# Optimization experiments

Measured on AMD Instinct MI355X. Metric: run time of the kernel, lower is better.

The kernel has to match this reference:

```python
import jax, jax.numpy as jnp
import numpy as np

B = 128                      # num_graphs (cell lines per batch)
SIZES = [706, 512, 256, 128] # nodes per graph at each level; final_node = 128
DIM = 256                    # dim_cell
DEG = 8                      # avg degree of gene-gene network
EPS = 1e-5                   # BatchNorm eps


def _build_graph():
    """Build per-graph edges (incl. self-loops, as GATConv adds) and predefined
    cluster assignments per layer, coarsening edges exactly like PyG max_pool
    (remove self-loops + coalesce). Replicated across B graphs with offsets."""
    rng = np.random.default_rng(0)
    e = rng.integers(0, SIZES[0], size=(2, SIZES[0] * DEG))
    e = e[:, e[0] != e[1]]
    e = np.unique(e, axis=1)
    edges, clusters = [], []
    cur = e
    for i in range(3):
        n_cur, n_next = SIZES[i], SIZES[i + 1]
        sl = np.arange(n_cur)
        e_sl = np.concatenate([cur, np.stack([sl, sl])], axis=1)  # add self-loops
        off = np.arange(B) * n_cur
        eg = (e_sl[:, None, :] + off[None, :, None]).reshape(2, -1)
        edges.append(eg.astype(np.int32))
        cl = np.concatenate([np.arange(n_next), rng.integers(0, n_next, size=n_cur - n_next)])
        rng.shuffle(cl)  # surjective cluster assignment n_cur -> n_next
        clg = (cl[None, :] + (np.arange(B) * n_next)[:, None]).reshape(-1)
        clusters.append(clg.astype(np.int32))
        src, dst = cl[cur[0]], cl[cur[1]]
        m = src != dst                      # pool_edge: remove self-loops
        cur = np.unique(np.stack([src[m], dst[m]]), axis=1)  # coalesce
    return edges, clusters


def setup_inputs() -> dict:
    edges, clusters = _build_graph()
    key = jax.random.key(0)
    ks = jax.random.split(key, 16)
    d = {"x": jax.random.normal(ks[0], (B * SIZES[0], 3), jnp.float32)}
    ins = [3, DIM, DIM]
    for i in range(3):
        s = 1.0 / np.sqrt(ins[i])
        a = 1.0 / np.sqrt(DIM)
        d[f"W{i}"] = jax.random.normal(ks[1 + i], (ins[i], DIM), jnp.float32) * s
        d[f"asrc{i}"] = jax.random.normal(ks[4 + i], (DIM,), jnp.float32) * a
        d[f"adst{i}"] = jax.random.normal(ks[7 + i], (DIM,), jnp.float32) * a
        d[f"b{i}"] = jnp.zeros((DIM,), jnp.float32)
        d[f"edge{i}"] = jnp.asarray(edges[i])
        d[f"cluster{i}"] = jnp.asarray(clusters[i])
    return d


def _gat(x, edge, W, a_s, a_d, b):
    """PyG GATConv, heads=1, negative_slope=0.2 (self-loops pre-added in edge)."""
    N = x.shape[0]
    h = x @ W                                    # [N, D]
    src, dst = edge[0], edge[1]
    e = jax.nn.leaky_relu((h * a_s).sum(-1)[src] + (h * a_d).sum(-1)[dst], 0.2)
    m = jax.ops.segment_max(e, dst, num_segments=N)     # segment softmax (stable)
    ex = jnp.exp(e - m[dst])
    ssum = jax.ops.segment_sum(ex, dst, num_segments=N)
    alpha = ex / ssum[dst]
    out = jax.ops.segment_sum(h[src] * alpha[:, None], dst, num_segments=N)
    return out + b


def _forward(x, Ws, a_ss, a_ds, bs, edges, clusters):
    for i in range(3):
        x = jax.nn.relu(_gat(x, edges[i], Ws[i], a_ss[i], a_ds[i], bs[i]))
        # max_pool: scatter-max over predefined clusters (coarsen nodes)
        x = jax.ops.segment_max(x, clusters[i], num_segments=B * SIZES[i + 1])
        # BatchNorm1d(affine=False), training mode: biased batch stats
        mean = x.mean(0)
        var = x.var(0)
        x = (x - mean) * jax.lax.rsqrt(var + EPS)
    return x.reshape(B, SIZES[3] * DIM)


def reference(x, W0, W1, W2, asrc0, asrc1, asrc2, adst0, adst1, adst2,
              b0, b1, b2, edge0, edge1, edge2, cluster0, cluster1, cluster2):
    return _forward(x, (W0, W1, W2), (asrc0, asrc1, asrc2), (adst0, adst1, adst2),
                    (b0, b1, b2), (edge0, edge1, edge2), (cluster0, cluster1, cluster2))
```

## Files before the change

kernel.cpp:

```cpp
#include <hip/hip_runtime.h>
#include <hip/hip_fp16.h>

#define DIM 256
#define MAXMEM 16
#define MAXDEG 288

typedef _Float16 f16x8 __attribute__((ext_vector_type(8)));
typedef float f32x4 __attribute__((ext_vector_type(4)));

__device__ inline unsigned short f2h(float f) {
  return __half_as_ushort(__float2half_rn(f));
}
__device__ inline float h2f(unsigned short u) {
  return __half2float(__ushort_as_half(u));
}
__device__ inline __half2 hmax2_(__half2 a, __half2 b) {
  __half2 c;
  c.x = __hgt(a.x, b.x) ? a.x : b.x;
  c.y = __hgt(a.y, b.y) ? a.y : b.y;
  return c;
}


__global__ __launch_bounds__(256) void l0_fused(
    const float* __restrict__ x, const float* __restrict__ W,
    const float* __restrict__ asv, const float* __restrict__ adv,
    unsigned short* __restrict__ h, float* __restrict__ ssrc,
    float* __restrict__ sdst, int N, int Nb0) {
  int wid = (blockIdx.x * 256 + threadIdx.x) >> 6;
  int lane = threadIdx.x & 63;
  if (wid >= N) return;
  int nb = wid >> 7, g = wid & 127;
  const float* xr = x + ((size_t)g * Nb0 + nb) * 3;
  float x0 = xr[0], x1 = xr[1], x2 = xr[2];
  int c = lane * 4;
  float4 w0 = *(const float4*)(W + c);
  float4 w1 = *(const float4*)(W + 256 + c);
  float4 w2 = *(const float4*)(W + 512 + c);
  float4 hv;
  hv.x = fmaf(x0, w0.x, fmaf(x1, w1.x, x2 * w2.x));
  hv.y = fmaf(x0, w0.y, fmaf(x1, w1.y, x2 * w2.y));
  hv.z = fmaf(x0, w0.z, fmaf(x1, w1.z, x2 * w2.z));
  hv.w = fmaf(x0, w0.w, fmaf(x1, w1.w, x2 * w2.w));
  ((ushort4*)(h + (size_t)wid * DIM))[lane] =
      make_ushort4(f2h(hv.x), f2h(hv.y), f2h(hv.z), f2h(hv.w));
  float4 a1 = ((const float4*)asv)[lane];
  float4 a2 = ((const float4*)adv)[lane];
  float d1 = hv.x * a1.x + hv.y * a1.y + hv.z * a1.z + hv.w * a1.w;
  float d2 = hv.x * a2.x + hv.y * a2.y + hv.z * a2.z + hv.w * a2.w;
  for (int o = 32; o > 0; o >>= 1) {
    d1 += __shfl_down(d1, o);
    d2 += __shfl_down(d2, o);
  }
  if (lane == 0) { ssrc[wid] = d1; sdst[wid] = d2; }
}

__global__ __launch_bounds__(256) void prep_k(
    const float* __restrict__ W, const float* __restrict__ sums,
    const float* __restrict__ sqs, float invN,
    unsigned short* __restrict__ Wt, float* __restrict__ cvec) {
  int n = blockIdx.x;
  int k = threadIdx.x;
  float mu = sums[k] * invN;
  float var = sqs[k] * invN - mu * mu;
  float istd = rsqrtf(var + 1e-5f);
  float w = W[(size_t)k * 256 + n] * istd;
  Wt[(size_t)n * 256 + k] = f2h(w);
  __shared__ float red[256];
  red[k] = mu * w;
  __syncthreads();
  for (int s = 128; s > 0; s >>= 1) {
    if (k < s) red[k] += red[k + s];
    __syncthreads();
  }
  if (k == 0) cvec[n] = -red[0];
}

__global__ __launch_bounds__(256) void gemm_mfma(
    const unsigned short* __restrict__ A, const unsigned short* __restrict__ Wt,
    const float* __restrict__ cvec, const float* __restrict__ asv,
    const float* __restrict__ adv, unsigned short* __restrict__ H,
    float* __restrict__ ssrc, float* __restrict__ sdst, int M) {
  __shared__ unsigned short Bs[2][256 * 32];
  int tid = threadIdx.x;
  int wave = tid >> 6, lane = tid & 63;
  int m0 = blockIdx.x * 128 + wave * 32;
  int row = lane & 15, quad = lane >> 4;

#pragma unroll
  for (int i = 0; i < 4; i++) {
    int c = i * 256 + tid;
    f16x8 v = *(const f16x8*)(const void*)(Wt + (size_t)(c >> 2) * 256 + (c & 3) * 8);
    *(f16x8*)(void*)(&Bs[0][c * 8]) = v;
  }
  __syncthreads();

  const unsigned short* Ap = A + (size_t)(m0 + row) * 256 + quad * 8;
  f32x4 acc[2][16] = {};
  for (int j = 0; j < 8; j++) {
    f16x8 pf[4];
    if (j < 7) {
#pragma unroll
      for (int i = 0; i < 4; i++) {
        int c = i * 256 + tid;
        pf[i] = *(const f16x8*)(const void*)(Wt + (size_t)(c >> 2) * 256 +
                                             (j + 1) * 32 + (c & 3) * 8);
      }
    }
    f16x8 a0 = *(const f16x8*)(const void*)(Ap + j * 32);
    f16x8 a1 = *(const f16x8*)(const void*)(Ap + 16 * 256 + j * 32);
    const unsigned short* bs = Bs[j & 1];
#pragma unroll
    for (int nt = 0; nt < 16; nt++) {
      f16x8 b = *(const f16x8*)(const void*)(bs + (nt * 16 + row) * 32 + quad * 8);
      acc[0][nt] = __builtin_amdgcn_mfma_f32_16x16x32_f16(a0, b, acc[0][nt], 0, 0, 0);
      acc[1][nt] = __builtin_amdgcn_mfma_f32_16x16x32_f16(a1, b, acc[1][nt], 0, 0, 0);
    }
    if (j < 7) {
#pragma unroll
      for (int i = 0; i < 4; i++) {
        int c = i * 256 + tid;
        *(f16x8*)(void*)(&Bs[(j + 1) & 1][c * 8]) = pf[i];
      }
    }
    __syncthreads();
  }

  float sav[16], sdv[16], cv[16];
#pragma unroll
  for (int nt = 0; nt < 16; nt++) {
    sav[nt] = asv[nt * 16 + row];
    sdv[nt] = adv[nt * 16 + row];
    cv[nt] = cvec[nt * 16 + row];
  }
#pragma unroll
  for (int sub = 0; sub < 2; sub++)
#pragma unroll
    for (int r = 0; r < 4; r++) {
      int mm = m0 + sub * 16 + quad * 4 + r;
      unsigned short* out = H + (size_t)mm * 256 + row;
      float d1 = 0.f, d2 = 0.f;
#pragma unroll
      for (int nt = 0; nt < 16; nt++) {
        float hv = acc[sub][nt][r] + cv[nt];
        out[nt * 16] = f2h(hv);
        d1 = fmaf(hv, sav[nt], d1);
        d2 = fmaf(hv, sdv[nt], d2);
      }
      for (int o = 1; o < 16; o <<= 1) {
        d1 += __shfl_xor(d1, o);
        d2 += __shfl_xor(d2, o);
      }
      if (row == 0) { ssrc[mm] = d1; sdst[mm] = d2; }
    }
}

struct BktArgs {
  const int* esrc[3]; const int* edst[3]; const int* cl[3];
  int Eb[3]; int Nb[3]; int est[3];
  int* bdeg[3]; int* bccnt[3]; int* bebkt[3]; int* bcbkt[3];
};
__global__ void bucket3_k(BktArgs a) {
  int L = blockIdx.y;
  int i = blockIdx.x * 256 + threadIdx.x;
  if (i < a.Eb[L]) {
    int d = a.edst[L][i];
    int slot = atomicAdd(&a.bdeg[L][d], 1);
    if (slot < a.est[L]) a.bebkt[L][d * a.est[L] + slot] = a.esrc[L][i];
  }
  if (i < a.Nb[L]) {
    int c = a.cl[L][i];
    int slot = atomicAdd(&a.bccnt[L][c], 1);
    if (slot < MAXMEM) a.bcbkt[L][c * MAXMEM + slot] = i;
  }
}

__global__ __launch_bounds__(256) void gat_fused(
    const unsigned short* __restrict__ h, const int* __restrict__ bdeg,
    const int* __restrict__ bebkt, int estride,
    const int* __restrict__ bccnt, const int* __restrict__ bcbkt,
    const float* __restrict__ ssrc, const float* __restrict__ sdst,
    const float* __restrict__ bias, unsigned short* __restrict__ pooled,
    int Mb, int lgMb) {
  __shared__ float pLDS[MAXDEG * 8];
  __shared__ float psum[8];
  int b = blockIdx.x;
  int x = b & 7, t = b >> 3;
  int c = t & (Mb - 1);
  int set = x + 8 * (t >> lgMb);
  int tid = threadIdx.x;
  int gl = tid >> 5;
  int ch = tid & 31;
  int g = set * 8 + gl;
  int nm = bccnt[c]; if (nm > MAXMEM) nm = MAXMEM;
  float4 bf0 = *(const float4*)(bias + ch * 8);
  float4 bf1 = *(const float4*)(bias + ch * 8 + 4);
  __half2 hb[4] = {__floats2half2_rn(bf0.x, bf0.y), __floats2half2_rn(bf0.z, bf0.w),
                   __floats2half2_rn(bf1.x, bf1.y), __floats2half2_rn(bf1.z, bf1.w)};
  __half2 z = __float2half2_rn(0.f);
  __half2 best[4] = {z, z, z, z};
  for (int mi = 0; mi < nm; mi++) {
    int nb = __builtin_amdgcn_readfirstlane(bcbkt[c * MAXMEM + mi]);
    int deg = __builtin_amdgcn_readfirstlane(bdeg[nb]);
    if (deg > estride) deg = estride;
    const int* bk = bebkt + nb * estride;
    if (tid < 8) psum[tid] = 0.f;
    __syncthreads();
    for (int jj = tid; jj < deg * 8; jj += 256) {
      int j = jj >> 3, gi = jj & 7;
      int g2 = set * 8 + gi;
      int s = bk[j];
      float tt = ssrc[s * 128 + g2] + sdst[nb * 128 + g2];
      tt = tt > 0.f ? tt : 0.2f * tt;
      float p = __expf(tt);
      pLDS[jj] = p;
      atomicAdd(&psum[gi], p);
    }
    __syncthreads();
    float inv = 1.f / psum[gl];
    __half2 acc[4] = {z, z, z, z};
    int j = 0;
    for (; j + 4 <= deg; j += 4) {
      int4 ss = *(const int4*)(bk + j);
      __half2 hq0 = __float2half2_rn(pLDS[(j + 0) * 8 + gl] * inv);
      __half2 hq1 = __float2half2_rn(pLDS[(j + 1) * 8 + gl] * inv);
      __half2 hq2 = __float2half2_rn(pLDS[(j + 2) * 8 + gl] * inv);
      __half2 hq3 = __float2half2_rn(pLDS[(j + 3) * 8 + gl] * inv);
      uint4 v0 = *(const uint4*)(h + ((size_t)ss.x * 128 + g) * DIM + ch * 8);
      uint4 v1 = *(const uint4*)(h + ((size_t)ss.y * 128 + g) * DIM + ch * 8);
      uint4 v2 = *(const uint4*)(h + ((size_t)ss.z * 128 + g) * DIM + ch * 8);
      uint4 v3 = *(const uint4*)(h + ((size_t)ss.w * 128 + g) * DIM + ch * 8);
      union { uint4 u; __half2 p[4]; } u0, u1, u2, u3;
      u0.u = v0; u1.u = v1; u2.u = v2; u3.u = v3;
#pragma unroll
      for (int i = 0; i < 4; i++) {
        acc[i] = __hfma2(u0.p[i], hq0, acc[i]);
        acc[i] = __hfma2(u1.p[i], hq1, acc[i]);
        acc[i] = __hfma2(u2.p[i], hq2, acc[i]);
        acc[i] = __hfma2(u3.p[i], hq3, acc[i]);
      }
    }
    for (; j < deg; j++) {
      int s = bk[j];
      __half2 hq = __float2half2_rn(pLDS[j * 8 + gl] * inv);
      uint4 v0 = *(const uint4*)(h + ((size_t)s * 128 + g) * DIM + ch * 8);
      union { uint4 u; __half2 p[4]; } u0; u0.u = v0;
#pragma unroll
      for (int i = 0; i < 4; i++) acc[i] = __hfma2(u0.p[i], hq, acc[i]);
    }
#pragma unroll
    for (int i = 0; i < 4; i++)
      best[i] = hmax2_(best[i], __hadd2(acc[i], hb[i]));
    __syncthreads();
  }
  union { uint4 u; __half2 p[4]; } o;
#pragma unroll
  for (int i = 0; i < 4; i++) o.p[i] = best[i];
  *(uint4*)(pooled + ((size_t)c * 128 + g) * DIM + ch * 8) = o.u;
}

__global__ __launch_bounds__(256) void stats_k(
    const unsigned short* __restrict__ x, float* __restrict__ sums,
    float* __restrict__ sqs, int M) {
  int tid = threadIdx.x;
  int ch = tid & 31;
  int rg = tid >> 5;
  float s[8] = {}, q[8] = {};
  for (int r = blockIdx.x * 8 + rg; r < M; r += gridDim.x * 8) {
    uint4 v = *(const uint4*)(x + (size_t)r * DIM + ch * 8);
    union { uint4 u; __half2 p[4]; } uu; uu.u = v;
#pragma unroll
    for (int i = 0; i < 4; i++) {
      float2 f = __half22float2(uu.p[i]);
      s[2 * i]     += f.x; q[2 * i]     = fmaf(f.x, f.x, q[2 * i]);
      s[2 * i + 1] += f.y; q[2 * i + 1] = fmaf(f.y, f.y, q[2 * i + 1]);
    }
  }
  __shared__ float sm[512];
  sm[tid] = 0.f; sm[tid + 256] = 0.f;
  __syncthreads();
#pragma unroll
  for (int i = 0; i < 8; i++) {
    atomicAdd(&sm[ch * 8 + i], s[i]);
    atomicAdd(&sm[256 + ch * 8 + i], q[i]);
  }
  __syncthreads();
  atomicAdd(&sums[tid], sm[tid]);
  atomicAdd(&sqs[tid], sm[tid + 256]);
}

__global__ void norm_out(const unsigned short* __restrict__ xin,
                         float* __restrict__ xout,
                         const float* __restrict__ sums, const float* __restrict__ sqs,
                         float invN, int Mb, int total) {
  int idx = blockIdx.x * 256 + threadIdx.x;
  if (idx >= total) return;
  int ch = idx & 255;
  int r = idx >> 8;
  int g = r & 127, c = r >> 7;
  float mu = sums[ch] * invN;
  float var = sqs[ch] * invN - mu * mu;
  float v = (h2f(xin[idx]) - mu) * rsqrtf(var + 1e-5f);
  xout[((size_t)g * Mb + c) * 256 + ch] = v;
}

extern "C" void kernel_launch(void* const* d_in, const int* in_sizes, int n_in,
                              void* d_out, int out_size, void* d_ws, size_t ws_size,
                              hipStream_t stream) {
  const int B = 128;
  const int Nb[4] = {706, 512, 256, 128};
  const int Ns[4] = {128 * 706, 128 * 512, 128 * 256, 128 * 128};
  const int lgMb[3] = {9, 8, 7};
  const int EST[3] = {64, 160, 288};

  int iW[3], iA[3], iD[3], iB_[3], iE[3], iC[3];
  if (in_sizes[2] == 256) {
    for (int i = 0; i < 3; i++) {
      iW[i] = 1 + 6 * i; iA[i] = 2 + 6 * i; iD[i] = 3 + 6 * i;
      iB_[i] = 4 + 6 * i; iE[i] = 5 + 6 * i; iC[i] = 6 + 6 * i;
    }
  } else {
    for (int i = 0; i < 3; i++) {
      iW[i] = 1 + i; iA[i] = 4 + i; iD[i] = 7 + i;
      iB_[i] = 10 + i; iE[i] = 13 + i; iC[i] = 16 + i;
    }
  }
  int E[3];
  for (int i = 0; i < 3; i++) E[i] = in_sizes[iE[i]] / 2;

  int bebktOff[3], bcbktOff[3];
  size_t bebktTot = 0, bcbktTot = 0;
  for (int i = 0; i < 3; i++) {
    bebktOff[i] = (int)bebktTot; bebktTot += (size_t)Nb[i] * EST[i];
    bcbktOff[i] = (int)bcbktTot; bcbktTot += (size_t)Nb[i + 1] * MAXMEM;
  }

  char* wsp = (char*)d_ws;
  size_t o = 0;
  auto alloc = [&](size_t bytes) -> void* {
    void* p = wsp + o;
    o = (o + bytes + 255) & ~(size_t)255;
    return p;
  };
  unsigned short* h      = (unsigned short*)alloc((size_t)Ns[0] * DIM * 2);
  unsigned short* pooled = (unsigned short*)alloc((size_t)Ns[1] * DIM * 2);
  float* ssrc   = (float*)alloc((size_t)Ns[0] * 4);
  float* sdst   = (float*)alloc((size_t)Ns[0] * 4);
  float* statbuf= (float*)alloc(3 * 512 * 4);
  int*   bmeta  = (int*)alloc((size_t)3 * (Nb[0] + Nb[1]) * 4);
  char*  zend   = wsp + o;
  int*   bebkt  = (int*)alloc(bebktTot * 4);
  int*   bcbkt  = (int*)alloc(bcbktTot * 4);
  unsigned short* Wt = (unsigned short*)alloc(256 * 256 * 2);
  float* cvec   = (float*)alloc(256 * 4);
  (void)ws_size; (void)n_in; (void)out_size;

  const float* xin = (const float*)d_in[0];

  hipMemsetAsync(statbuf, 0, (size_t)(zend - (char*)statbuf), stream);

  BktArgs ba;
  int maxG = 0;
  for (int L = 0; L < 3; L++) {
    int Eb = E[L] / B;
    ba.esrc[L] = (const int*)d_in[iE[L]];
    ba.edst[L] = ba.esrc[L] + E[L];
    ba.cl[L]   = (const int*)d_in[iC[L]];
    ba.Eb[L] = Eb; ba.Nb[L] = Nb[L]; ba.est[L] = EST[L];
    ba.bdeg[L]  = bmeta + L * (Nb[0] + Nb[1]);
    ba.bccnt[L] = ba.bdeg[L] + Nb[L];
    ba.bebkt[L] = bebkt + bebktOff[L];
    ba.bcbkt[L] = bcbkt + bcbktOff[L];
    int gneed = (Eb > Nb[L] ? Eb : Nb[L]);
    if (gneed > maxG) maxG = gneed;
  }
  dim3 bg((maxG + 255) / 256, 3);
  bucket3_k<<<bg, 256, 0, stream>>>(ba);

  for (int L = 0; L < 3; L++) {
    int N = Ns[L], M = Ns[L + 1];
    int NbL = Nb[L];
    const float* W  = (const float*)d_in[iW[L]];
    const float* av = (const float*)d_in[iA[L]];
    const float* dv = (const float*)d_in[iD[L]];
    const float* bv = (const float*)d_in[iB_[L]];
    float* sums = statbuf + L * 512;
    float* sqs  = sums + 256;
    int* bdeg = bmeta + L * (Nb[0] + Nb[1]);
    int* bccnt = bdeg + NbL;
    int* beb = bebkt + bebktOff[L];
    int* bcb = bcbkt + bcbktOff[L];

    if (L == 0) {
      l0_fused<<<(N + 3) / 4, 256, 0, stream>>>(xin, W, av, dv, h, ssrc, sdst,
                                                N, NbL);
    } else {
      float* psums = statbuf + (L - 1) * 512;
      prep_k<<<256, 256, 0, stream>>>(W, psums, psums + 256, 1.0f / (float)N,
                                      Wt, cvec);
      gemm_mfma<<<N / 128, 256, 0, stream>>>(pooled, Wt, cvec, av, dv,
                                             h, ssrc, sdst, N);
    }

    int MbL = Nb[L + 1];
    gat_fused<<<MbL * 16, 256, 0, stream>>>(h, bdeg, beb, EST[L], bccnt, bcb,
                                            ssrc, sdst, bv, pooled,
                                            MbL, lgMb[L]);

    stats_k<<<512, 256, 0, stream>>>(pooled, sums, sqs, M);
  }

  norm_out<<<((size_t)Ns[3] * DIM + 255) / 256, 256, 0, stream>>>(
      pooled, (float*)d_out, statbuf + 2 * 512, statbuf + 2 * 512 + 256,
      1.0f / (float)Ns[3], Nb[3], Ns[3] * DIM);
}
```

Measured before the change: 348.7 us.

## Fuse BatchNorm statistics into gat_fused epilogue and drop stats kernel

```diff
diff --git a/kernel.cpp b/kernel.cpp
--- a/kernel.cpp
+++ b/kernel.cpp
@@ -56,21 +56,26 @@
 }
 
 __global__ __launch_bounds__(256) void prep_k(
-    const float* __restrict__ W, const float* __restrict__ sums,
-    const float* __restrict__ sqs, float invN,
-    unsigned short* __restrict__ Wt, float* __restrict__ cvec) {
+    const float* __restrict__ W, const float* __restrict__ stats,
+    float invN, unsigned short* __restrict__ Wt, float* __restrict__ cvec) {
   int n = blockIdx.x;
   int k = threadIdx.x;
-  float mu = sums[k] * invN;
-  float var = sqs[k] * invN - mu * mu;
+  float s = 0.f, q = 0.f;
+#pragma unroll
+  for (int r = 0; r < 8; r++) {
+    s += stats[r * 512 + k];
+    q += stats[r * 512 + 256 + k];
+  }
+  float mu = s * invN;
+  float var = q * invN - mu * mu;
   float istd = rsqrtf(var + 1e-5f);
   float w = W[(size_t)k * 256 + n] * istd;
   Wt[(size_t)n * 256 + k] = f2h(w);
   __shared__ float red[256];
   red[k] = mu * w;
   __syncthreads();
-  for (int s = 128; s > 0; s >>= 1) {
-    if (k < s) red[k] += red[k + s];
+  for (int sft = 128; sft > 0; sft >>= 1) {
+    if (k < sft) red[k] += red[k + sft];
     __syncthreads();
   }
   if (k == 0) cvec[n] = -red[0];
@@ -181,9 +186,10 @@
     const int* __restrict__ bccnt, const int* __restrict__ bcbkt,
     const float* __restrict__ ssrc, const float* __restrict__ sdst,
     const float* __restrict__ bias, unsigned short* __restrict__ pooled,
-    int Mb, int lgMb) {
+    float* __restrict__ stats, int Mb, int lgMb) {
   __shared__ float pLDS[MAXDEG * 8];
   __shared__ float psum[8];
+  __shared__ float sred[512];
   int b = blockIdx.x;
   int x = b & 7, t = b >> 3;
   int c = t & (Mb - 1);
@@ -192,6 +198,8 @@
   int gl = tid >> 5;
   int ch = tid & 31;
   int g = set * 8 + gl;
+  sred[tid] = 0.f;
+  sred[tid + 256] = 0.f;
   int nm = bccnt[c]; if (nm > MAXMEM) nm = MAXMEM;
   float4 bf0 = *(const float4*)(bias + ch * 8);
   float4 bf1 = *(const float4*)(bias + ch * 8 + 4);
@@ -199,6 +207,7 @@
                    __floats2half2_rn(bf1.x, bf1.y), __floats2half2_rn(bf1.z, bf1.w)};
   __half2 z = __float2half2_rn(0.f);
   __half2 best[4] = {z, z, z, z};
+  __syncthreads();
   for (int mi = 0; mi < nm; mi++) {
     int nb = __builtin_amdgcn_readfirstlane(bcbkt[c * MAXMEM + mi]);
     int deg = __builtin_amdgcn_readfirstlane(bdeg[nb]);
@@ -257,49 +266,37 @@
 #pragma unroll
   for (int i = 0; i < 4; i++) o.p[i] = best[i];
   *(uint4*)(pooled + ((size_t)c * 128 + g) * DIM + ch * 8) = o.u;
-}
-
-__global__ __launch_bounds__(256) void stats_k(
-    const unsigned short* __restrict__ x, float* __restrict__ sums,
-    float* __restrict__ sqs, int M) {
-  int tid = threadIdx.x;
-  int ch = tid & 31;
-  int rg = tid >> 5;
-  float s[8] = {}, q[8] = {};
-  for (int r = blockIdx.x * 8 + rg; r < M; r += gridDim.x * 8) {
-    uint4 v = *(const uint4*)(x + (size_t)r * DIM + ch * 8);
-    union { uint4 u; __half2 p[4]; } uu; uu.u = v;
-#pragma unroll
-    for (int i = 0; i < 4; i++) {
-      float2 f = __half22float2(uu.p[i]);
-      s[2 * i]     += f.x; q[2 * i]     = fmaf(f.x, f.x, q[2 * i]);
-      s[2 * i + 1] += f.y; q[2 * i + 1] = fmaf(f.y, f.y, q[2 * i + 1]);
-    }
-  }
-  __shared__ float sm[512];
-  sm[tid] = 0.f; sm[tid + 256] = 0.f;
+#pragma unroll
+  for (int i = 0; i < 4; i++) {
+    float2 f = __half22float2(best[i]);
+    atomicAdd(&sred[ch * 8 + 2 * i], f.x);
+    atomicAdd(&sred[ch * 8 + 2 * i + 1], f.y);
+    atomicAdd(&sred[256 + ch * 8 + 2 * i], f.x * f.x);
+    atomicAdd(&sred[256 + ch * 8 + 2 * i + 1], f.y * f.y);
+  }
   __syncthreads();
-#pragma unroll
-  for (int i = 0; i < 8; i++) {
-    atomicAdd(&sm[ch * 8 + i], s[i]);
-    atomicAdd(&sm[256 + ch * 8 + i], q[i]);
-  }
-  __syncthreads();
-  atomicAdd(&sums[tid], sm[tid]);
-  atomicAdd(&sqs[tid], sm[tid + 256]);
+  float* sg = stats + (b & 7) * 512;
+  atomicAdd(&sg[tid], sred[tid]);
+  atomicAdd(&sg[tid + 256], sred[tid + 256]);
 }
 
 __global__ void norm_out(const unsigned short* __restrict__ xin,
                          float* __restrict__ xout,
-                         const float* __restrict__ sums, const float* __restrict__ sqs,
+                         const float* __restrict__ stats,
                          float invN, int Mb, int total) {
   int idx = blockIdx.x * 256 + threadIdx.x;
   if (idx >= total) return;
   int ch = idx & 255;
   int r = idx >> 8;
   int g = r & 127, c = r >> 7;
-  float mu = sums[ch] * invN;
-  float var = sqs[ch] * invN - mu * mu;
+  float s = 0.f, q = 0.f;
+#pragma unroll
+  for (int rr = 0; rr < 8; rr++) {
+    s += stats[rr * 512 + ch];
+    q += stats[rr * 512 + 256 + ch];
+  }
+  float mu = s * invN;
+  float var = q * invN - mu * mu;
   float v = (h2f(xin[idx]) - mu) * rsqrtf(var + 1e-5f);
   xout[((size_t)g * Mb + c) * 256 + ch] = v;
 }
@@ -346,7 +343,7 @@
   unsigned short* pooled = (unsigned short*)alloc((size_t)Ns[1] * DIM * 2);
   float* ssrc   = (float*)alloc((size_t)Ns[0] * 4);
   float* sdst   = (float*)alloc((size_t)Ns[0] * 4);
-  float* statbuf= (float*)alloc(3 * 512 * 4);
+  float* statbuf= (float*)alloc((size_t)3 * 8 * 512 * 4);
   int*   bmeta  = (int*)alloc((size_t)3 * (Nb[0] + Nb[1]) * 4);
   char*  zend   = wsp + o;
   int*   bebkt  = (int*)alloc(bebktTot * 4);
@@ -378,14 +375,13 @@
   bucket3_k<<<bg, 256, 0, stream>>>(ba);
 
   for (int L = 0; L < 3; L++) {
-    int N = Ns[L], M = Ns[L + 1];
+    int N = Ns[L];
     int NbL = Nb[L];
     const float* W  = (const float*)d_in[iW[L]];
     const float* av = (const float*)d_in[iA[L]];
     const float* dv = (const float*)d_in[iD[L]];
     const float* bv = (const float*)d_in[iB_[L]];
-    float* sums = statbuf + L * 512;
-    float* sqs  = sums + 256;
+    float* statL = statbuf + (size_t)L * 8 * 512;
     int* bdeg = bmeta + L * (Nb[0] + Nb[1]);
     int* bccnt = bdeg + NbL;
     int* beb = bebkt + bebktOff[L];
@@ -395,22 +391,19 @@
       l0_fused<<<(N + 3) / 4, 256, 0, stream>>>(xin, W, av, dv, h, ssrc, sdst,
                                                 N, NbL);
     } else {
-      float* psums = statbuf + (L - 1) * 512;
-      prep_k<<<256, 256, 0, stream>>>(W, psums, psums + 256, 1.0f / (float)N,
-                                      Wt, cvec);
+      float* psums = statbuf + (size_t)(L - 1) * 8 * 512;
+      prep_k<<<256, 256, 0, stream>>>(W, psums, 1.0f / (float)N, Wt, cvec);
       gemm_mfma<<<N / 128, 256, 0, stream>>>(pooled, Wt, cvec, av, dv,
                                              h, ssrc, sdst, N);
     }
 
     int MbL = Nb[L + 1];
     gat_fused<<<MbL * 16, 256, 0, stream>>>(h, bdeg, beb, EST[L], bccnt, bcb,
-                                            ssrc, sdst, bv, pooled,
+                                            ssrc, sdst, bv, pooled, statL,
                                             MbL, lgMb[L]);
-
-    stats_k<<<512, 256, 0, stream>>>(pooled, sums, sqs, M);
   }
 
   norm_out<<<((size_t)Ns[3] * DIM + 255) / 256, 256, 0, stream>>>(
-      pooled, (float*)d_out, statbuf + 2 * 512, statbuf + 2 * 512 + 256,
+      pooled, (float*)d_out, statbuf + (size_t)2 * 8 * 512,
       1.0f / (float)Ns[3], Nb[3], Ns[3] * DIM);
 }
```

Measured after the change: 566.1 us. 62.3% more time.
